# Performance work log

Measured on AMD Instinct MI355X. Metric: run time of the kernel, lower is better.

The kernel has to match this reference:

```python
import jax, jax.numpy as jnp
import numpy as np

H = 1024
NH = 16
DK = H // NH
FF = 4 * H
EPS = 1e-5

def layer_norm(x, g, b):
    mu = jnp.mean(x, axis=-1, keepdims=True)
    var = jnp.mean(jnp.square(x - mu), axis=-1, keepdims=True)
    return (x - mu) * jax.lax.rsqrt(var + EPS) * g + b

def setup_inputs() -> dict:
    key = jax.random.key(0)
    ks = jax.random.split(key, 12)
    s = 0.02
    return {
        "x": jax.random.normal(ks[0], (2, 2048, H), dtype=jnp.float32),
        "ln_g": jnp.ones((H,), jnp.float32),
        "ln_b": jnp.zeros((H,), jnp.float32),
        "wq": jax.random.normal(ks[1], (H, H), jnp.float32) * s,
        "bq": jnp.zeros((H,), jnp.float32),
        "wk": jax.random.normal(ks[2], (H, H), jnp.float32) * s,
        "bk": jnp.zeros((H,), jnp.float32),
        "wv": jax.random.normal(ks[3], (H, H), jnp.float32) * s,
        "bv": jnp.zeros((H,), jnp.float32),
        "w1": jax.random.normal(ks[4], (H, FF), jnp.float32) * s,
        "b1": jnp.zeros((FF,), jnp.float32),
        "w2": jax.random.normal(ks[5], (FF, H), jnp.float32) * s,
        "b2": jnp.zeros((H,), jnp.float32),
    }

def reference(x, ln_g, ln_b, wq, bq, wk, bk, wv, bv, w1, b1, w2, b2):
    B, S, _ = x.shape
    # Note: the torch module reuses the SAME LayerNorm params for both norms.
    h = layer_norm(x, ln_g, ln_b)
    q = (h @ wq + bq).reshape(B, S, NH, DK).transpose(0, 2, 1, 3)  # [B,NH,S,DK]
    k = (h @ wk + bk).reshape(B, S, NH, DK).transpose(0, 2, 1, 3)
    v = (h @ wv + bv).reshape(B, S, NH, DK).transpose(0, 2, 1, 3)
    scores = jnp.einsum('bhqd,bhkd->bhqk', q, k) / jnp.sqrt(jnp.float32(DK))
    att = jax.nn.softmax(scores, axis=-1)  # [B,NH,S,S]
    att_out = jnp.einsum('bhqk,bhkd->bhqd', att, v)
    att_out = att_out.transpose(0, 2, 1, 3).reshape(B, S, H)
    x = x + att_out  # dropout_prob=0 -> identity
    h2 = layer_norm(x, ln_g, ln_b)
    mlp = jax.nn.gelu(h2 @ w1 + b1, approximate=False) @ w2 + b2
    x = x + mlp
    return (x, att)
```

## Files before the change

kernel.cpp:

```cpp
#include <hip/hip_runtime.h>
#include <hip/hip_bf16.h>

typedef unsigned short u16;
typedef __attribute__((ext_vector_type(8))) short short8;
typedef __attribute__((ext_vector_type(4))) float f32x4;
typedef __attribute__((ext_vector_type(4))) unsigned int u32x4;

__device__ inline u16 f2bf(float f) {
    unsigned int u = __float_as_uint(f);
    unsigned int r = (u + 0x7fffu + ((u >> 16) & 1u)) >> 16;
    return (u16)r;
}

__device__ __forceinline__ void gload16(const u16* g, u16* l) {
    __builtin_amdgcn_global_load_lds(
        (const __attribute__((address_space(1))) void*)g,
        (__attribute__((address_space(3))) void*)l, 16, 0, 0);
}

__global__ void transpose_cvt(const float* __restrict__ in, u16* __restrict__ out,
                              int K, int N) {
    __shared__ float tile[32][33];
    int n0 = blockIdx.x * 32, k0 = blockIdx.y * 32;
    int tx = threadIdx.x, ty = threadIdx.y;
#pragma unroll
    for (int i = 0; i < 4; i++)
        tile[ty + i * 8][tx] = in[(size_t)(k0 + ty + i * 8) * N + n0 + tx];
    __syncthreads();
#pragma unroll
    for (int i = 0; i < 4; i++)
        out[(size_t)(n0 + ty + i * 8) * K + k0 + tx] = f2bf(tile[tx][ty + i * 8]);
}

template <bool ADD>
__global__ void ln_kernel(const float* __restrict__ x, const float* __restrict__ add,
                          const float* __restrict__ g, const float* __restrict__ b,
                          float* __restrict__ xa_out, u16* __restrict__ h_out) {
    int row = blockIdx.x;
    int t = threadIdx.x;
    float4 v = ((const float4*)(x + (size_t)row * 1024))[t];
    if (ADD) {
        float4 a = ((const float4*)(add + (size_t)row * 1024))[t];
        v.x += a.x; v.y += a.y; v.z += a.z; v.w += a.w;
        ((float4*)(xa_out + (size_t)row * 1024))[t] = v;
    }
    float s = v.x + v.y + v.z + v.w;
    float sq = v.x * v.x + v.y * v.y + v.z * v.z + v.w * v.w;
#pragma unroll
    for (int off = 32; off >= 1; off >>= 1) {
        s  += __shfl_xor(s, off);
        sq += __shfl_xor(sq, off);
    }
    __shared__ float ps[4], pq[4];
    int wid = t >> 6, lane = t & 63;
    if (lane == 0) { ps[wid] = s; pq[wid] = sq; }
    __syncthreads();
    s  = ps[0] + ps[1] + ps[2] + ps[3];
    sq = pq[0] + pq[1] + pq[2] + pq[3];
    float mu  = s * (1.0f / 1024.0f);
    float var = sq * (1.0f / 1024.0f) - mu * mu;
    float rstd = rsqrtf(var + 1e-5f);
    float4 gv = ((const float4*)g)[t];
    float4 bv = ((const float4*)b)[t];
    ushort4 o;
    o.x = f2bf((v.x - mu) * rstd * gv.x + bv.x);
    o.y = f2bf((v.y - mu) * rstd * gv.y + bv.y);
    o.z = f2bf((v.z - mu) * rstd * gv.z + bv.z);
    o.w = f2bf((v.w - mu) * rstd * gv.w + bv.w);
    ((ushort4*)(h_out + (size_t)row * 1024))[t] = o;
}

__device__ __forceinline__ void xcd_swizzle(int BN, int& m0, int& n0) {
    int gx = gridDim.x;
    int lin = blockIdx.x + gx * blockIdx.y;
    int cpx = (gx * gridDim.y) >> 3;
    int swz = (lin & 7) * cpx + (lin >> 3);
    n0 = (swz % gx) * BN;
    m0 = (swz / gx) * 128;
}

template <int BN>
__device__ __forceinline__ void gemm_core(
    const u16* __restrict__ A, const u16* __restrict__ Bt, int K,
    int m0, int n0, u16* As, u16* Bs, f32x4 (*acc)[BN / 32]) {
    const int NB = BN / 32;
    int t = threadIdx.x, lane = t & 63, w = t >> 6;
    int l15 = lane & 15, lhi = lane >> 4;
    int wm = (w >> 1) * 64, wn = (w & 1) * (BN / 2);

    int srow8 = (lane >> 3) & 7;
    int scol = ((lane & 7) ^ srow8) * 8;
    const u16* Ag = A + (size_t)(m0 + w * 32 + (lane >> 3)) * K + scol;
    const u16* Bg = Bt + (size_t)(n0 + w * (BN / 4) + (lane >> 3)) * K + scol;
    u16* AsW = As + (w * 32) * 64;
    u16* BsW = Bs + (w * (BN / 4)) * 64;

    int rs = (l15 & 7) << 3;

    for (int k0 = 0; k0 < K; k0 += 64) {
        __syncthreads();
#pragma unroll
        for (int j = 0; j < 4; j++)
            gload16(Ag + k0 + (size_t)j * 8 * K, AsW + j * 8 * 64);
#pragma unroll
        for (int j = 0; j < NB; j++)
            gload16(Bg + k0 + (size_t)j * 8 * K, BsW + j * 8 * 64);
        __syncthreads();
#pragma unroll
        for (int ks = 0; ks < 2; ks++) {
            short8 af[4], bfr[NB];
#pragma unroll
            for (int mi = 0; mi < 4; mi++)
                af[mi] = *(const short8*)&As[(wm + mi * 16 + l15) * 64 +
                                             ((ks * 32 + lhi * 8) ^ rs)];
#pragma unroll
            for (int ni = 0; ni < NB; ni++)
                bfr[ni] = *(const short8*)&Bs[(wn + ni * 16 + l15) * 64 +
                                              ((ks * 32 + lhi * 8) ^ rs)];
#pragma unroll
            for (int mi = 0; mi < 4; mi++)
#pragma unroll
                for (int ni = 0; ni < NB; ni++)
                    acc[mi][ni] = __builtin_amdgcn_mfma_f32_16x16x32_bf16(
                        af[mi], bfr[ni], acc[mi][ni], 0, 0, 0);
        }
    }
}

__global__ __launch_bounds__(256) void qkv_gemm(
    const u16* __restrict__ A,
    const u16* __restrict__ wqT, const u16* __restrict__ wkT, const u16* __restrict__ wvT,
    const float* __restrict__ bq, const float* __restrict__ bk, const float* __restrict__ bv,
    u16* __restrict__ qb, u16* __restrict__ kb, u16* __restrict__ vtb) {
    __shared__ alignas(16) u16 As[128 * 64];
    __shared__ alignas(16) u16 Bs[128 * 64];
    int z = blockIdx.z;
    const u16* Bt = z == 0 ? wqT : (z == 1 ? wkT : wvT);
    const float* bias = z == 0 ? bq : (z == 1 ? bk : bv);
    float scale = z == 0 ? 0.18033688011112042f : 1.0f;
    int m0, n0;
    xcd_swizzle(128, m0, n0);

    f32x4 acc[4][4] = {};
    gemm_core<128>(A, Bt, 1024, m0, n0, As, Bs, acc);

    int t = threadIdx.x, lane = t & 63, w = t >> 6;
    int l15 = lane & 15, lhi = lane >> 4;
    int wm = (w >> 1) * 64, wn = (w & 1) * 64;
#pragma unroll
    for (int mi = 0; mi < 4; mi++)
#pragma unroll
        for (int ni = 0; ni < 4; ni++)
#pragma unroll
            for (int r = 0; r < 4; r++) {
                int row = m0 + wm + mi * 16 + lhi * 4 + r;
                int col = n0 + wn + ni * 16 + l15;
                u16 o = f2bf((acc[mi][ni][r] + bias[col]) * scale);
                int bb = row >> 11, ss = row & 2047, hh = col >> 6, dd = col & 63;
                if (z < 2) {
                    u16* outp = z == 0 ? qb : kb;
                    outp[(((size_t)(bb * 16 + hh) * 2048) + ss) * 64 + dd] = o;
                } else {
                    vtb[(((size_t)(bb * 16 + hh) * 64) + dd) * 2048 + ss] = o;
                }
            }
}

template <int MODE, int BN>
__global__ __launch_bounds__(256) void mlp_gemm(
    const u16* __restrict__ A, const u16* __restrict__ Bt,
    const float* __restrict__ bias, void* __restrict__ outp,
    const float* __restrict__ resid, int N, int K) {
    __shared__ alignas(16) u16 As[128 * 64];
    __shared__ alignas(16) u16 Bs[BN * 64];
    int m0, n0;
    xcd_swizzle(BN, m0, n0);

    f32x4 acc[4][BN / 32] = {};
    gemm_core<BN>(A, Bt, K, m0, n0, As, Bs, acc);

    int t = threadIdx.x, lane = t & 63, w = t >> 6;
    int l15 = lane & 15, lhi = lane >> 4;
    int wm = (w >> 1) * 64, wn = (w & 1) * (BN / 2);
#pragma unroll
    for (int mi = 0; mi < 4; mi++)
#pragma unroll
        for (int ni = 0; ni < BN / 32; ni++)
#pragma unroll
            for (int r = 0; r < 4; r++) {
                int row = m0 + wm + mi * 16 + lhi * 4 + r;
                int col = n0 + wn + ni * 16 + l15;
                float val = acc[mi][ni][r] + bias[col];
                if (MODE == 2) {
                    float gl = 0.5f * val * (1.0f + erff(val * 0.70710678118654752f));
                    ((u16*)outp)[(size_t)row * N + col] = f2bf(gl);
                } else {
                    ((float*)outp)[(size_t)row * N + col] =
                        val + resid[(size_t)row * N + col];
                }
            }
}

__global__ __launch_bounds__(512) void attn_kernel(
    const u16* __restrict__ q, const u16* __restrict__ k,
    const u16* __restrict__ vt, float* __restrict__ att,
    float* __restrict__ attout) {
    const int S = 2048;
    int bx = blockIdx.x;
    int swz = (bx & 7) * 64 + (bx >> 3);
    int bh = swz >> 4;
    int qb = swz & 15;
    int t = threadIdx.x, w = t >> 6, lane = t & 63;
    int l15 = lane & 15, lhi = lane >> 4;
    int q0 = qb * 128 + w * 16;

    const u16* qh = q + (size_t)bh * S * 64;
    const u16* kh = k + (size_t)bh * S * 64;
    const u16* vh = vt + (size_t)bh * 64 * S;

    __shared__ alignas(16) u16 Ks[2][64][64];
    __shared__ alignas(16) u16 Vs[2][64][64];

    int srow = lane >> 3;
    int scol = (((lane & 7) ^ srow)) * 8;
    const u16* kg = kh + (size_t)(w * 8 + srow) * 64 + scol;
    const u16* vg = vh + (size_t)(w * 8 + srow) * 2048 + scol;
    u16* ksl[2] = {&Ks[0][w * 8][0], &Ks[1][w * 8][0]};
    u16* vsl[2] = {&Vs[0][w * 8][0], &Vs[1][w * 8][0]};

    short8 aq0 = *(const short8*)&qh[(size_t)(q0 + l15) * 64 + lhi * 8];
    short8 aq1 = *(const short8*)&qh[(size_t)(q0 + l15) * 64 + 32 + lhi * 8];

    f32x4 z = {0.f, 0.f, 0.f, 0.f};
    float sum = 0.f;

    gload16(kg, ksl[0]);
    for (int i = 0; i < 32; i++) {
        __syncthreads();
        if (i + 1 < 32) gload16(kg + (size_t)(i + 1) * 64 * 64, ksl[(i + 1) & 1]);
        const u16(*Kb)[64] = Ks[i & 1];
#pragma unroll
        for (int sub = 0; sub < 4; sub++) {
            int R = sub * 16 + l15;
            int cs = (R & 7) << 3;
            short8 b0 = *(const short8*)&Kb[R][(lhi * 8) ^ cs];
            short8 b1 = *(const short8*)&Kb[R][(32 + lhi * 8) ^ cs];
            f32x4 s = z;
            s = __builtin_amdgcn_mfma_f32_16x16x32_bf16(b0, aq0, s, 0, 0, 0);
            s = __builtin_amdgcn_mfma_f32_16x16x32_bf16(b1, aq1, s, 0, 0, 0);
            sum += __builtin_exp2f(s[0]) + __builtin_exp2f(s[1]) +
                   __builtin_exp2f(s[2]) + __builtin_exp2f(s[3]);
        }
    }
    sum += __shfl_xor(sum, 16);
    sum += __shfl_xor(sum, 32);
    float lrl = -__log2f(sum);

    f32x4 o[4];
#pragma unroll
    for (int ni = 0; ni < 4; ni++) o[ni] = z;

    float* attq = att + ((size_t)bh * S + q0) * S;

    gload16(kg, ksl[0]);
    gload16(vg, vsl[0]);
    for (int i = 0; i < 32; i++) {
        __syncthreads();
        if (i + 1 < 32) {
            gload16(kg + (size_t)(i + 1) * 64 * 64, ksl[(i + 1) & 1]);
            gload16(vg + (i + 1) * 64, vsl[(i + 1) & 1]);
        }
        const u16(*Kb)[64] = Ks[i & 1];
        const u16(*Vb)[64] = Vs[i & 1];
#pragma unroll
        for (int kp2 = 0; kp2 < 2; kp2++) {
            int ktb = i * 64 + kp2 * 32;
            unsigned int v0, v1, v2, v3;
#pragma unroll
            for (int half = 0; half < 2; half++) {
                int R = kp2 * 32 + half * 16 + l15;
                int cs = (R & 7) << 3;
                short8 kb0 = *(const short8*)&Kb[R][(lhi * 8) ^ cs];
                short8 kb1 = *(const short8*)&Kb[R][(32 + lhi * 8) ^ cs];
                f32x4 s = {lrl, lrl, lrl, lrl};
                s = __builtin_amdgcn_mfma_f32_16x16x32_bf16(kb0, aq0, s, 0, 0, 0);
                s = __builtin_amdgcn_mfma_f32_16x16x32_bf16(kb1, aq1, s, 0, 0, 0);
                f32x4 p;
#pragma unroll
                for (int r = 0; r < 4; r++) p[r] = __builtin_exp2f(s[r]);
                *(f32x4*)&attq[(size_t)l15 * S + ktb + half * 16 + lhi * 4] = p;
                unsigned int lo = (unsigned int)f2bf(p[0]) |
                                  ((unsigned int)f2bf(p[1]) << 16);
                unsigned int hi = (unsigned int)f2bf(p[2]) |
                                  ((unsigned int)f2bf(p[3]) << 16);
                if (half == 0) { v0 = lo; v1 = hi; } else { v2 = lo; v3 = hi; }
            }
            int srcA = l15 + (((lhi * 2) & 3) << 4);
            int srcB = srcA + 16;
            unsigned int a0 = (unsigned int)__shfl((int)v0, srcA);
            unsigned int a1 = (unsigned int)__shfl((int)v1, srcA);
            unsigned int bb0 = (unsigned int)__shfl((int)v0, srcB);
            unsigned int bb1 = (unsigned int)__shfl((int)v1, srcB);
            unsigned int c0 = (unsigned int)__shfl((int)v2, srcA);
            unsigned int c1 = (unsigned int)__shfl((int)v3, srcA);
            unsigned int d0 = (unsigned int)__shfl((int)v2, srcB);
            unsigned int d1 = (unsigned int)__shfl((int)v3, srcB);
            bool hw = lhi >= 2;
            u32x4 wv;
            wv[0] = hw ? c0 : a0;
            wv[1] = hw ? c1 : a1;
            wv[2] = hw ? d0 : bb0;
            wv[3] = hw ? d1 : bb1;
            short8 pa = __builtin_bit_cast(short8, wv);
#pragma unroll
            for (int ni = 0; ni < 4; ni++) {
                int R = ni * 16 + l15;
                int cs = (R & 7) << 3;
                short8 vb = *(const short8*)&Vb[R][(kp2 * 32 + lhi * 8) ^ cs];
                o[ni] = __builtin_amdgcn_mfma_f32_16x16x32_bf16(pa, vb, o[ni], 0, 0, 0);
            }
        }
    }

    int bb = bh >> 4, hh = bh & 15;
#pragma unroll
    for (int ni = 0; ni < 4; ni++)
#pragma unroll
        for (int r = 0; r < 4; r++) {
            int srw = q0 + lhi * 4 + r;
            attout[((size_t)(bb * 2048 + srw)) * 1024 + hh * 64 + ni * 16 + l15] = o[ni][r];
        }
}

extern "C" void kernel_launch(void* const* d_in, const int* in_sizes, int n_in,
                              void* d_out, int out_size, void* d_ws, size_t ws_size,
                              hipStream_t stream) {
    const float* x    = (const float*)d_in[0];
    const float* ln_g = (const float*)d_in[1];
    const float* ln_b = (const float*)d_in[2];
    const float* wq   = (const float*)d_in[3];
    const float* bq   = (const float*)d_in[4];
    const float* wk   = (const float*)d_in[5];
    const float* bk   = (const float*)d_in[6];
    const float* wv   = (const float*)d_in[7];
    const float* bv   = (const float*)d_in[8];
    const float* w1   = (const float*)d_in[9];
    const float* b1   = (const float*)d_in[10];
    const float* w2   = (const float*)d_in[11];
    const float* b2   = (const float*)d_in[12];

    char* ws = (char*)d_ws;
    const size_t MB = 1024 * 1024;
    u16* wqT = (u16*)(ws + 0 * MB);
    u16* wkT = (u16*)(ws + 2 * MB);
    u16* wvT = (u16*)(ws + 4 * MB);
    u16* w1T = (u16*)(ws + 6 * MB);
    u16* w2T = (u16*)(ws + 14 * MB);
    u16* h1  = (u16*)(ws + 22 * MB);
    u16* qb  = (u16*)(ws + 30 * MB);
    u16* kb  = (u16*)(ws + 38 * MB);
    u16* vtb = (u16*)(ws + 46 * MB);
    u16* ub  = (u16*)(ws + 22 * MB);
    float* attout = (float*)(ws + 54 * MB);
    float* xa = (float*)(ws + 70 * MB);
    u16* h2  = (u16*)(ws + 86 * MB);

    float* xout = (float*)d_out;
    float* att  = xout + (size_t)2 * 2048 * 1024;

    dim3 tb(32, 8);
    transpose_cvt<<<dim3(32, 32), tb, 0, stream>>>(wq, wqT, 1024, 1024);
    transpose_cvt<<<dim3(32, 32), tb, 0, stream>>>(wk, wkT, 1024, 1024);
    transpose_cvt<<<dim3(32, 32), tb, 0, stream>>>(wv, wvT, 1024, 1024);
    transpose_cvt<<<dim3(128, 32), tb, 0, stream>>>(w1, w1T, 1024, 4096);
    transpose_cvt<<<dim3(32, 128), tb, 0, stream>>>(w2, w2T, 4096, 1024);

    ln_kernel<false><<<4096, 256, 0, stream>>>(x, nullptr, ln_g, ln_b, nullptr, h1);

    qkv_gemm<<<dim3(8, 32, 3), 256, 0, stream>>>(h1, wqT, wkT, wvT, bq, bk, bv,
                                                 qb, kb, vtb);

    attn_kernel<<<512, 512, 0, stream>>>(qb, kb, vtb, att, attout);

    ln_kernel<true><<<4096, 256, 0, stream>>>(x, attout, ln_g, ln_b, xa, h2);

    mlp_gemm<2, 128><<<dim3(32, 32), 256, 0, stream>>>(h2, w1T, b1, ub, nullptr, 4096, 1024);
    mlp_gemm<3, 64><<<dim3(16, 32), 256, 0, stream>>>(ub, w2T, b2, xout, xa, 1024, 4096);
}
```

Measured before the change: 428.9 us.

## Merge QKV weight transposes, drop XCD swizzle, widen down-proj GEMM tile

Combines the three QKV weight transpose launches into one kernel using blockIdx.z. Removes the XCD-aware block swizzle from the GEMMs and uses plain row-major tile mapping. Changes the MLP down-projection GEMM from a 64-wide to a 128-wide N tile, halving its grid to 256 blocks. The wider tile improves operand reuse, but fewer blocks may underfill the GPU on the K=4096 GEMM, and dropping the swizzle may lower L2 locality.

```diff
diff --git a/kernel.cpp b/kernel.cpp
--- a/kernel.cpp
+++ b/kernel.cpp
@@ -16,6 +16,25 @@
     __builtin_amdgcn_global_load_lds(
         (const __attribute__((address_space(1))) void*)g,
         (__attribute__((address_space(3))) void*)l, 16, 0, 0);
+}
+
+__global__ void transpose_cvt3(const float* __restrict__ in0, u16* __restrict__ out0,
+                               const float* __restrict__ in1, u16* __restrict__ out1,
+                               const float* __restrict__ in2, u16* __restrict__ out2) {
+    const int K = 1024, N = 1024;
+    int z = blockIdx.z;
+    const float* in = z == 0 ? in0 : (z == 1 ? in1 : in2);
+    u16* out = z == 0 ? out0 : (z == 1 ? out1 : out2);
+    __shared__ float tile[32][33];
+    int n0 = blockIdx.x * 32, k0 = blockIdx.y * 32;
+    int tx = threadIdx.x, ty = threadIdx.y;
+#pragma unroll
+    for (int i = 0; i < 4; i++)
+        tile[ty + i * 8][tx] = in[(size_t)(k0 + ty + i * 8) * N + n0 + tx];
+    __syncthreads();
+#pragma unroll
+    for (int i = 0; i < 4; i++)
+        out[(size_t)(n0 + ty + i * 8) * K + k0 + tx] = f2bf(tile[tx][ty + i * 8]);
 }
 
 __global__ void transpose_cvt(const float* __restrict__ in, u16* __restrict__ out,
@@ -70,15 +89,6 @@
     ((ushort4*)(h_out + (size_t)row * 1024))[t] = o;
 }
 
-__device__ __forceinline__ void xcd_swizzle(int BN, int& m0, int& n0) {
-    int gx = gridDim.x;
-    int lin = blockIdx.x + gx * blockIdx.y;
-    int cpx = (gx * gridDim.y) >> 3;
-    int swz = (lin & 7) * cpx + (lin >> 3);
-    n0 = (swz % gx) * BN;
-    m0 = (swz / gx) * 128;
-}
-
 template <int BN>
 __device__ __forceinline__ void gemm_core(
     const u16* __restrict__ A, const u16* __restrict__ Bt, int K,
@@ -138,8 +148,7 @@
     const u16* Bt = z == 0 ? wqT : (z == 1 ? wkT : wvT);
     const float* bias = z == 0 ? bq : (z == 1 ? bk : bv);
     float scale = z == 0 ? 0.18033688011112042f : 1.0f;
-    int m0, n0;
-    xcd_swizzle(128, m0, n0);
+    int n0 = blockIdx.x * 128, m0 = blockIdx.y * 128;
 
     f32x4 acc[4][4] = {};
     gemm_core<128>(A, Bt, 1024, m0, n0, As, Bs, acc);
@@ -173,8 +182,7 @@
     const float* __restrict__ resid, int N, int K) {
     __shared__ alignas(16) u16 As[128 * 64];
     __shared__ alignas(16) u16 Bs[BN * 64];
-    int m0, n0;
-    xcd_swizzle(BN, m0, n0);
+    int n0 = blockIdx.x * BN, m0 = blockIdx.y * 128;
 
     f32x4 acc[4][BN / 32] = {};
     gemm_core<BN>(A, Bt, K, m0, n0, As, Bs, acc);
@@ -369,9 +377,7 @@
     float* att  = xout + (size_t)2 * 2048 * 1024;
 
     dim3 tb(32, 8);
-    transpose_cvt<<<dim3(32, 32), tb, 0, stream>>>(wq, wqT, 1024, 1024);
-    transpose_cvt<<<dim3(32, 32), tb, 0, stream>>>(wk, wkT, 1024, 1024);
-    transpose_cvt<<<dim3(32, 32), tb, 0, stream>>>(wv, wvT, 1024, 1024);
+    transpose_cvt3<<<dim3(32, 32, 3), tb, 0, stream>>>(wq, wqT, wk, wkT, wv, wvT);
     transpose_cvt<<<dim3(128, 32), tb, 0, stream>>>(w1, w1T, 1024, 4096);
     transpose_cvt<<<dim3(32, 128), tb, 0, stream>>>(w2, w2T, 4096, 1024);
 
@@ -385,5 +391,5 @@
     ln_kernel<true><<<4096, 256, 0, stream>>>(x, attout, ln_g, ln_b, xa, h2);
 
     mlp_gemm<2, 128><<<dim3(32, 32), 256, 0, stream>>>(h2, w1T, b1, ub, nullptr, 4096, 1024);
-    mlp_gemm<3, 64><<<dim3(16, 32), 256, 0, stream>>>(ub, w2T, b2, xout, xa, 1024, 4096);
-}
+    mlp_gemm<3, 128><<<dim3(8, 32), 256, 0, stream>>>(ub, w2T, b2, xout, xa, 1024, 4096);
+}
```

Result: slower. 461.3 us (+7.5%).
